# Kernel optimization log

Hardware: AMD Instinct MI355X
Metric: run time of the kernel (lower is better)

The kernel has to match this reference:

```python
import jax, jax.numpy as jnp
import numpy as np

C = 6.5  # ALCOVE specificity constant

BATCH, NE, NDIMS = 2048, 2048, 128


def setup_inputs() -> dict:
    key = jax.random.key(0)
    k1, k2, k3 = jax.random.split(key, 3)
    inputs = jax.random.normal(k1, (BATCH, NDIMS), dtype=jnp.float32)
    exemplars = jax.random.normal(k2, (NE, NDIMS), dtype=jnp.float32)
    # attn initialized to ones/ndims in the original; use positive random values
    # scaled similarly so the exp argument stays in a reasonable range.
    attn = jax.random.uniform(k3, (NDIMS,), dtype=jnp.float32) / float(NDIMS)
    return {"inputs": inputs, "exemplars": exemplars, "attn": attn}


def reference(inputs, exemplars, attn):
    # Vectorized form of: exp(-c * sum_d attn_d * |exemplars - x|) per example.
    # diff: (batch, ne, ndims)
    diff = jnp.abs(exemplars[None, :, :] - inputs[:, None, :])
    dist = jnp.einsum('bed,d->be', diff, attn)  # weighted L1 distance
    return jnp.exp(-C * dist)  # (batch, ne)
```

## Files before the change

kernel.cpp:

```cpp
#include <hip/hip_runtime.h>
#include <hip/hip_fp16.h>
#include <stdint.h>


#define ND 128
#define NEC 2048
#define CCONST 6.5f

#define AAH(acc, x, e)                                              \
  {                                                                 \
    uint32_t t_;                                                    \
    asm("v_pk_add_f16 %0, %1, %2 neg_lo:[0,1] neg_hi:[0,1]"         \
        : "=v"(t_) : "v"(x), "v"(e));                               \
    t_ &= 0x7fff7fffu;                                              \
    asm("v_pk_add_f16 %0, %0, %1" : "+v"(acc) : "v"(t_));           \
  }

static __device__ __forceinline__ uint32_t pkh(float lo, float hi) {
  __half2 h = __floats2half2_rn(lo, hi);
  union { __half2 h; uint32_t u; } cv;
  cv.h = h;
  return cv.u;
}

static __device__ __forceinline__ float hsum(uint32_t u) {
  union { uint32_t u; __half2 h; } cv;
  cv.u = u;
  return __half2float(__low2half(cv.h)) + __half2float(__high2half(cv.h));
}

__global__ __launch_bounds__(256, 4)
void alcove_rbf_kernel(const float* __restrict__ X,
                       const float* __restrict__ E,
                       const float* __restrict__ A,
                       float* __restrict__ out) {
  __shared__ uint32_t Eh[64 * 64];
  __shared__ uint32_t Xh[64 * 64];

  const int tid = threadIdx.x;
  const int e0 = blockIdx.x * 64;
  const int b0 = blockIdx.y * 64;

  {
    const int r = tid & 63;
    const int g = tid >> 6;
    const float4* Ap = reinterpret_cast<const float4*>(A + 32 * g);
    const float4* Ep = reinterpret_cast<const float4*>(E + (size_t)(e0 + r) * ND + 32 * g);
    const float4* Xp = reinterpret_cast<const float4*>(X + (size_t)(b0 + r) * ND + 32 * g);
#pragma unroll
    for (int k = 0; k < 8; ++k) {
      float4 a = Ap[k];
      float4 ev = Ep[k];
      float4 xv = Xp[k];
      int dd = 16 * g + 2 * k;
      Eh[dd * 64 + r]       = pkh(ev.x * a.x, ev.y * a.y);
      Eh[(dd + 1) * 64 + r] = pkh(ev.z * a.z, ev.w * a.w);
      Xh[dd * 64 + r]       = pkh(xv.x * a.x, xv.y * a.y);
      Xh[(dd + 1) * 64 + r] = pkh(xv.z * a.z, xv.w * a.w);
    }
  }
  __syncthreads();

  const int lane = tid & 63;
  const int w = tid >> 6;
  const int el = lane & 15;
  const int xg = lane >> 4;

  uint32_t acc[4][4];
#pragma unroll
  for (int j = 0; j < 4; ++j)
#pragma unroll
    for (int i = 0; i < 4; ++i) acc[j][i] = 0u;

  const uint4* Ev = reinterpret_cast<const uint4*>(Eh);
  const uint4* Xv = reinterpret_cast<const uint4*>(Xh);
  const int xoff = 4 * w + xg;

#pragma unroll 8
  for (int dd = 0; dd < 64; ++dd) {
    uint4 ev = Ev[dd * 16 + el];
    uint4 xv = Xv[dd * 16 + xoff];
    AAH(acc[0][0], xv.x, ev.x); AAH(acc[0][1], xv.x, ev.y);
    AAH(acc[0][2], xv.x, ev.z); AAH(acc[0][3], xv.x, ev.w);
    AAH(acc[1][0], xv.y, ev.x); AAH(acc[1][1], xv.y, ev.y);
    AAH(acc[1][2], xv.y, ev.z); AAH(acc[1][3], xv.y, ev.w);
    AAH(acc[2][0], xv.z, ev.x); AAH(acc[2][1], xv.z, ev.y);
    AAH(acc[2][2], xv.z, ev.z); AAH(acc[2][3], xv.z, ev.w);
    AAH(acc[3][0], xv.w, ev.x); AAH(acc[3][1], xv.w, ev.y);
    AAH(acc[3][2], xv.w, ev.z); AAH(acc[3][3], xv.w, ev.w);
  }

#pragma unroll
  for (int j = 0; j < 4; ++j) {
    int b = b0 + 16 * w + 4 * xg + j;
    float4 o;
    o.x = __expf(-CCONST * hsum(acc[j][0]));
    o.y = __expf(-CCONST * hsum(acc[j][1]));
    o.z = __expf(-CCONST * hsum(acc[j][2]));
    o.w = __expf(-CCONST * hsum(acc[j][3]));
    reinterpret_cast<float4*>(out + (size_t)b * NEC + e0)[el] = o;
  }
}

extern "C" void kernel_launch(void* const* d_in, const int* in_sizes, int n_in,
                              void* d_out, int out_size, void* d_ws, size_t ws_size,
                              hipStream_t stream) {
  const float* X = (const float*)d_in[0];
  const float* E = (const float*)d_in[1];
  const float* A = (const float*)d_in[2];
  float* out = (float*)d_out;

  dim3 grid(NEC / 64, 2048 / 64);
  dim3 block(256);
  alcove_rbf_kernel<<<grid, block, 0, stream>>>(X, E, A, out);
}
```

Baseline: 91.37 us.

## Accumulate L1 distance in fp32 from fp16-staged tiles instead of packed fp16

Replaces the packed fp16 subtract/abs/add inline-asm inner loop with unpacking the fp16 operands to fp32 and accumulating the absolute differences in fp32. It also changes the global load mapping so four consecutive threads read one row, and simplifies the thread-to-output mapping. The main intent appears to be accuracy: fp16 accumulation over 128 dims risks error. The cost is that each tile pair now needs conversions plus scalar fp32 sub/abs/add per element instead of packed ops, roughly doubling ALU work in the hot loop.

```diff
diff --git a/kernel.cpp b/kernel.cpp
--- a/kernel.cpp
+++ b/kernel.cpp
@@ -7,26 +7,16 @@
 #define NEC 2048
 #define CCONST 6.5f
 
-#define AAH(acc, x, e)                                              \
-  {                                                                 \
-    uint32_t t_;                                                    \
-    asm("v_pk_add_f16 %0, %1, %2 neg_lo:[0,1] neg_hi:[0,1]"         \
-        : "=v"(t_) : "v"(x), "v"(e));                               \
-    t_ &= 0x7fff7fffu;                                              \
-    asm("v_pk_add_f16 %0, %0, %1" : "+v"(acc) : "v"(t_));           \
-  }
-
-static __device__ __forceinline__ uint32_t pkh(float lo, float hi) {
-  __half2 h = __floats2half2_rn(lo, hi);
+static __device__ __forceinline__ uint32_t pack2(float lo, float hi) {
   union { __half2 h; uint32_t u; } cv;
-  cv.h = h;
+  cv.h = __floats2half2_rn(lo, hi);
   return cv.u;
 }
 
-static __device__ __forceinline__ float hsum(uint32_t u) {
+static __device__ __forceinline__ float2 unp2(uint32_t u) {
   union { uint32_t u; __half2 h; } cv;
   cv.u = u;
-  return __half2float(__low2half(cv.h)) + __half2float(__high2half(cv.h));
+  return __half22float2(cv.h);
 }
 
 __global__ __launch_bounds__(256, 4)
@@ -34,71 +24,70 @@
                        const float* __restrict__ E,
                        const float* __restrict__ A,
                        float* __restrict__ out) {
-  __shared__ uint32_t Eh[64 * 64];
-  __shared__ uint32_t Xh[64 * 64];
+  __shared__ __align__(16) uint32_t Eh[64 * 64];
+  __shared__ __align__(16) uint32_t Xh[64 * 64];
 
   const int tid = threadIdx.x;
   const int e0 = blockIdx.x * 64;
   const int b0 = blockIdx.y * 64;
 
   {
-    const int r = tid & 63;
-    const int g = tid >> 6;
-    const float4* Ap = reinterpret_cast<const float4*>(A + 32 * g);
-    const float4* Ep = reinterpret_cast<const float4*>(E + (size_t)(e0 + r) * ND + 32 * g);
-    const float4* Xp = reinterpret_cast<const float4*>(X + (size_t)(b0 + r) * ND + 32 * g);
+    const int lane_in = tid & 3;
+    const int r = tid >> 2;
+    const float4* Ap = reinterpret_cast<const float4*>(A);
+    const float4* Xp = reinterpret_cast<const float4*>(X + (size_t)(b0 + r) * ND);
+    const float4* Ep = reinterpret_cast<const float4*>(E + (size_t)(e0 + r) * ND);
 #pragma unroll
     for (int k = 0; k < 8; ++k) {
-      float4 a = Ap[k];
-      float4 ev = Ep[k];
-      float4 xv = Xp[k];
-      int dd = 16 * g + 2 * k;
-      Eh[dd * 64 + r]       = pkh(ev.x * a.x, ev.y * a.y);
-      Eh[(dd + 1) * 64 + r] = pkh(ev.z * a.z, ev.w * a.w);
-      Xh[dd * 64 + r]       = pkh(xv.x * a.x, xv.y * a.y);
-      Xh[(dd + 1) * 64 + r] = pkh(xv.z * a.z, xv.w * a.w);
+      int c4 = 4 * k + lane_in;
+      float4 a = Ap[c4];
+      float4 xv = Xp[c4];
+      float4 ev = Ep[c4];
+      int dd = 2 * c4;
+      Xh[(dd + 0) * 64 + r] = pack2(xv.x * a.x, xv.y * a.y);
+      Xh[(dd + 1) * 64 + r] = pack2(xv.z * a.z, xv.w * a.w);
+      Eh[(dd + 0) * 64 + r] = pack2(ev.x * a.x, ev.y * a.y);
+      Eh[(dd + 1) * 64 + r] = pack2(ev.z * a.z, ev.w * a.w);
     }
   }
   __syncthreads();
 
-  const int lane = tid & 63;
-  const int w = tid >> 6;
-  const int el = lane & 15;
-  const int xg = lane >> 4;
+  const int tx = tid & 15;
+  const int ty = tid >> 4;
 
-  uint32_t acc[4][4];
+  float acc[4][4];
 #pragma unroll
   for (int j = 0; j < 4; ++j)
 #pragma unroll
-    for (int i = 0; i < 4; ++i) acc[j][i] = 0u;
+    for (int i = 0; i < 4; ++i) acc[j][i] = 0.f;
 
   const uint4* Ev = reinterpret_cast<const uint4*>(Eh);
   const uint4* Xv = reinterpret_cast<const uint4*>(Xh);
-  const int xoff = 4 * w + xg;
 
-#pragma unroll 8
+#pragma unroll 4
   for (int dd = 0; dd < 64; ++dd) {
-    uint4 ev = Ev[dd * 16 + el];
-    uint4 xv = Xv[dd * 16 + xoff];
-    AAH(acc[0][0], xv.x, ev.x); AAH(acc[0][1], xv.x, ev.y);
-    AAH(acc[0][2], xv.x, ev.z); AAH(acc[0][3], xv.x, ev.w);
-    AAH(acc[1][0], xv.y, ev.x); AAH(acc[1][1], xv.y, ev.y);
-    AAH(acc[1][2], xv.y, ev.z); AAH(acc[1][3], xv.y, ev.w);
-    AAH(acc[2][0], xv.z, ev.x); AAH(acc[2][1], xv.z, ev.y);
-    AAH(acc[2][2], xv.z, ev.z); AAH(acc[2][3], xv.z, ev.w);
-    AAH(acc[3][0], xv.w, ev.x); AAH(acc[3][1], xv.w, ev.y);
-    AAH(acc[3][2], xv.w, ev.z); AAH(acc[3][3], xv.w, ev.w);
+    uint4 eu = Ev[dd * 16 + tx];
+    uint4 xu = Xv[dd * 16 + ty];
+    float2 fe[4], fb[4];
+    fe[0] = unp2(eu.x); fe[1] = unp2(eu.y); fe[2] = unp2(eu.z); fe[3] = unp2(eu.w);
+    fb[0] = unp2(xu.x); fb[1] = unp2(xu.y); fb[2] = unp2(xu.z); fb[3] = unp2(xu.w);
+#pragma unroll
+    for (int j = 0; j < 4; ++j)
+#pragma unroll
+      for (int i = 0; i < 4; ++i) {
+        acc[j][i] += fabsf(fb[j].x - fe[i].x) + fabsf(fb[j].y - fe[i].y);
+      }
   }
 
 #pragma unroll
   for (int j = 0; j < 4; ++j) {
-    int b = b0 + 16 * w + 4 * xg + j;
+    int b = b0 + 4 * ty + j;
     float4 o;
-    o.x = __expf(-CCONST * hsum(acc[j][0]));
-    o.y = __expf(-CCONST * hsum(acc[j][1]));
-    o.z = __expf(-CCONST * hsum(acc[j][2]));
-    o.w = __expf(-CCONST * hsum(acc[j][3]));
-    reinterpret_cast<float4*>(out + (size_t)b * NEC + e0)[el] = o;
+    o.x = __expf(-CCONST * acc[j][0]);
+    o.y = __expf(-CCONST * acc[j][1]);
+    o.z = __expf(-CCONST * acc[j][2]);
+    o.w = __expf(-CCONST * acc[j][3]);
+    reinterpret_cast<float4*>(out + (size_t)b * NEC + e0)[tx] = o;
   }
 }
 
```

New measurement: 102.3 us. 1.12x slower.
